# Optimization experiments

Hardware: AMD Instinct MI355X
Metric: run time of the kernel (lower is better)

The kernel has to match this reference:

```python
import jax, jax.numpy as jnp
import numpy as np

N_SEQ, N_RES, C_M = 512, 256, 256
C_OUTER, C_Z = 32, 128
LN_EPS = 1e-5
NORM_EPS = 1e-3


def setup_inputs() -> dict:
    key = jax.random.key(0)
    ks = jax.random.split(key, 6)
    f32 = jnp.float32
    return {
        "act": jax.random.normal(ks[0], (N_SEQ, N_RES, C_M), f32),
        "mask": jnp.ones((N_SEQ, N_RES), f32),
        # LayerNorm params (create_scale=True, create_offset=True)
        "ln_scale": jnp.ones((C_M,), f32),
        "ln_offset": jnp.zeros((C_M,), f32),
        # left/right projections, 'linear' (VarianceScaling fan_in scale=1)
        "left_w": (jax.random.normal(ks[1], (C_M, C_OUTER), f32) / np.float32(np.sqrt(C_M))),
        "left_b": jnp.zeros((C_OUTER,), f32),
        "right_w": (jax.random.normal(ks[2], (C_M, C_OUTER), f32) / np.float32(np.sqrt(C_M))),
        "right_b": jnp.zeros((C_OUTER,), f32),
        # output_w: VarianceScaling(scale=2.0, fan_in) over (c_outer, c_outer) input dims
        "output_w": (jax.random.normal(ks[3], (C_OUTER, C_OUTER, C_Z), f32)
                     * np.float32(np.sqrt(2.0 / (C_OUTER * C_OUTER)))),
        "output_b": jnp.zeros((C_Z,), f32),
    }


def reference(act, mask, ln_scale, ln_offset, left_w, left_b, right_w, right_b,
              output_w, output_b):
    # LayerNorm over last axis
    mu = jnp.mean(act, axis=-1, keepdims=True)
    var = jnp.var(act, axis=-1, keepdims=True)
    x = (act - mu) * jax.lax.rsqrt(var + LN_EPS) * ln_scale + ln_offset

    m = mask[..., None]  # [N_seq, N_res, 1]
    left = m * (jnp.einsum('abm,mc->abc', x, left_w) + left_b)    # [A,B,Co]
    right = m * (jnp.einsum('abm,me->abe', x, right_w) + right_b)  # [A,D,Co]

    # mean outer product: sum over MSA depth a -> [B, D, Co, Co]
    op = jnp.einsum('abc,ade->bdce', left, right)
    out = jnp.einsum('bdce,cef->bdf', op, output_w) + output_b  # [B, D, Cz]

    # normalization by pairwise mask counts
    norm = jnp.einsum('ab,ad->bd', mask, mask)[..., None]  # [B, D, 1]
    return out / (NORM_EPS + norm)
```

## Files before the change

### kernel.cpp

```cpp
#include <hip/hip_runtime.h>
#include <hip/hip_bf16.h>
#include <stdint.h>

typedef short bf16x8 __attribute__((ext_vector_type(8)));
typedef float f32x4 __attribute__((ext_vector_type(4)));
typedef unsigned short u16x4 __attribute__((ext_vector_type(4)));
typedef unsigned short u16x8 __attribute__((ext_vector_type(8)));

#define GLOAD16(g, l) __builtin_amdgcn_global_load_lds( \
    (const __attribute__((address_space(1))) void*)(g), \
    (__attribute__((address_space(3))) void*)(l), 16, 0, 0)

__device__ __forceinline__ unsigned short f2bf(float f) {
  unsigned u = __float_as_uint(f);
  unsigned r = (u + 0x7fffu + ((u >> 16) & 1u)) >> 16;
  return (unsigned short)r;
}

__global__ __launch_bounds__(256) void prep_norm_k(
    const float* __restrict__ lw, const float* __restrict__ rw,
    const float* __restrict__ ow, const float* __restrict__ mask,
    unsigned short* __restrict__ Wt, unsigned short* __restrict__ wfragG,
    float* __restrict__ nrm) {
  const int bid = blockIdx.x;
  if (bid < 512) {
    int idx = bid * 256 + threadIdx.x;
    if (idx < 131072) {
      int f = idx >> 10, k2 = idx & 1023;
      int e = k2 >> 5, c = k2 & 31;
      Wt[idx] = f2bf(ow[(size_t)((c << 5) + e) * 128 + f]);
    }
    if (idx < 16384) {
      int frag = idx >> 9, lane = (idx >> 3) & 63, j = idx & 7;
      int wc = frag >> 4, ni = (frag >> 3) & 1, kk = frag & 7;
      int mrow = lane & 15, g = lane >> 4;
      int c = wc * 32 + ni * 16 + mrow;
      int k = kk * 32 + g * 8 + j;
      wfragG[idx] = f2bf(c < 32 ? lw[k * 32 + c] : rw[k * 32 + (c - 32)]);
    }
  } else {
    const int b = bid - 512, d = threadIdx.x;
    float s = 0.f;
    #pragma unroll 8
    for (int a = 0; a < 512; ++a)
      s += mask[a * 256 + b] * mask[a * 256 + d];
    nrm[(b << 8) + d] = s;
  }
}

__global__ __launch_bounds__(256, 4) void ln_proj(
    const float* __restrict__ act, const float* __restrict__ mask,
    const float* __restrict__ lns, const float* __restrict__ lno,
    const float* __restrict__ lb, const float* __restrict__ rb,
    const unsigned short* __restrict__ wfragG,
    unsigned short* __restrict__ Lt, unsigned short* __restrict__ Rt) {
  __shared__ char smem[32768];
  const int tid = threadIdx.x;
  const int lane = tid & 63;
  const int w = tid >> 6;
  const int b = blockIdx.y;
  const int a0 = blockIdx.x << 6;
  const int l = tid & 15;
  const int rg = tid >> 4;

  f32x4 sc[4], of[4];
  #pragma unroll
  for (int j = 0; j < 4; ++j) {
    sc[j] = *(const f32x4*)(lns + (l << 4) + (j << 2));
    of[j] = *(const f32x4*)(lno + (l << 4) + (j << 2));
  }

  #pragma unroll
  for (int i = 0; i < 4; ++i) {
    const int r = rg + (i << 4);
    const float* src = act + ((size_t)(a0 + r) * 256 + b) * 256 + (l << 4);
    f32x4 xv[4];
    #pragma unroll
    for (int j = 0; j < 4; ++j) xv[j] = *(const f32x4*)(src + (j << 2));
    float s = 0.f, sq = 0.f;
    #pragma unroll
    for (int j = 0; j < 4; ++j) {
      f32x4 v = xv[j];
      s += v[0] + v[1] + v[2] + v[3];
      sq += v[0] * v[0] + v[1] * v[1] + v[2] * v[2] + v[3] * v[3];
    }
    s += __shfl_xor(s, 1); sq += __shfl_xor(sq, 1);
    s += __shfl_xor(s, 2); sq += __shfl_xor(sq, 2);
    s += __shfl_xor(s, 4); sq += __shfl_xor(sq, 4);
    s += __shfl_xor(s, 8); sq += __shfl_xor(sq, 8);
    const float mu = s * (1.f / 256.f);
    const float rs = rsqrtf(sq * (1.f / 256.f) - mu * mu + 1e-5f);
    #pragma unroll
    for (int hh = 0; hh < 2; ++hh) {
      u16x8 pk;
      #pragma unroll
      for (int j2 = 0; j2 < 2; ++j2) {
        const int j = (hh << 1) + j2;
        #pragma unroll
        for (int e = 0; e < 4; ++e)
          pk[(j2 << 2) + e] = f2bf((xv[j][e] - mu) * rs * sc[j][e] + of[j][e]);
      }
      const int c = (l << 1) + hh;
      *(u16x8*)(smem + (r << 9) + ((c ^ (r & 7)) << 4)) = pk;
    }
  }
  __syncthreads();

  const int wr = w >> 1, wc = w & 1;
  const int mrow = lane & 15, g = lane >> 4;
  f32x4 acc[2][2];
  #pragma unroll
  for (int i = 0; i < 2; ++i)
    #pragma unroll
    for (int jj = 0; jj < 2; ++jj) acc[i][jj] = (f32x4){0.f, 0.f, 0.f, 0.f};
  #pragma unroll
  for (int kk = 0; kk < 8; ++kk) {
    bf16x8 af[2], bfr[2];
    #pragma unroll
    for (int mi = 0; mi < 2; ++mi) {
      const int row = (wr << 5) + (mi << 4) + mrow;
      af[mi] = *(const bf16x8*)(smem + (row << 9) + ((((kk << 2) + g) ^ (row & 7)) << 4));
    }
    #pragma unroll
    for (int ni = 0; ni < 2; ++ni)
      bfr[ni] = *(const bf16x8*)(wfragG + (size_t)((((wc << 1) + ni) << 3) + kk) * 512 + (lane << 3));
    #pragma unroll
    for (int mi = 0; mi < 2; ++mi)
      #pragma unroll
      for (int ni = 0; ni < 2; ++ni)
        acc[mi][ni] = __builtin_amdgcn_mfma_f32_16x16x32_bf16(af[mi], bfr[ni], acc[mi][ni], 0, 0, 0);
  }
  __syncthreads();

  #pragma unroll
  for (int ni = 0; ni < 2; ++ni) {
    const int c = (wc << 5) + (ni << 4) + mrow;
    const float bias = (wc == 0) ? lb[(ni << 4) + mrow] : rb[(ni << 4) + mrow];
    #pragma unroll
    for (int mi = 0; mi < 2; ++mi) {
      const int aB = (wr << 5) + (mi << 4) + (g << 2);
      u16x4 pk;
      #pragma unroll
      for (int qq = 0; qq < 4; ++qq) {
        const float mk = mask[(size_t)(a0 + aB + qq) * 256 + b];
        pk[qq] = f2bf((acc[mi][ni][qq] + bias) * mk);
      }
      *(u16x4*)(smem + (c << 7) + ((((aB >> 3) & 7) ^ (c & 7)) << 4) + ((aB & 7) << 1)) = pk;
    }
  }
  __syncthreads();

  #pragma unroll
  for (int s = 0; s < 2; ++s) {
    const int c = (w << 4) + (s << 3) + (lane >> 3);
    const int gr = lane & 7;
    const u16x8 v = *(const u16x8*)(smem + (c << 7) + ((gr ^ (c & 7)) << 4));
    unsigned short* dst = (c < 32) ? Lt : Rt;
    *(u16x8*)(dst + (size_t)(b * 32 + (c & 31)) * 512 + a0 + (gr << 3)) = v;
  }
}

__global__ __launch_bounds__(512, 2) void gemm_fused(
    const unsigned short* __restrict__ Lt, const unsigned short* __restrict__ Rt,
    const unsigned short* __restrict__ Wt, const float* __restrict__ nrm,
    const float* __restrict__ outb, float* __restrict__ out) {
  __shared__ char smem[131072];
  const int tid = threadIdx.x;
  const int lane = tid & 63;
  const int w = tid >> 6;
  const int wr = w >> 2, wc = w & 3;
  const int mrow = lane & 15, g = lane >> 4;

  const int bid = blockIdx.x;
  const int xcd = bid & 7, jj_ = bid >> 3;
  const int mb = ((jj_ >> 5) << 3) | (jj_ & 7);
  const int nb = (xcd << 2) | ((jj_ >> 3) & 3);
  const int m0i = mb << 8, n0i = nb << 8;

  const int scol = (((tid & 7) ^ ((tid >> 3) & 7)) << 3);

  f32x4 acc[8][4];
  #pragma unroll
  for (int i = 0; i < 8; ++i)
    #pragma unroll
    for (int jj = 0; jj < 4; ++jj) acc[i][jj] = (f32x4){0.f, 0.f, 0.f, 0.f};

  auto STG = [&](const unsigned short* gsrc, int baserow, int dstoff, int kt) {
    GLOAD16(gsrc + ((size_t)(baserow + (tid >> 3)) << 9) + (kt << 6) + scol,
            smem + dstoff + (tid << 4));
  };
  auto STGALL = [&](int buf, int kt) {
    STG(Rt, n0i, buf + 32768, kt);        STG(Rt, n0i + 64, buf + 40960, kt);
    STG(Rt, n0i + 128, buf + 49152, kt);  STG(Rt, n0i + 192, buf + 57344, kt);
    STG(Lt, m0i, buf + 0, kt);            STG(Lt, m0i + 64, buf + 8192, kt);
    STG(Lt, m0i + 128, buf + 16384, kt);  STG(Lt, m0i + 192, buf + 24576, kt);
  };

  STGALL(0, 0);
  STGALL(65536, 1);
  asm volatile("s_waitcnt vmcnt(8)" ::: "memory");
  __builtin_amdgcn_s_barrier();

  #pragma unroll 1
  for (int t = 0; t < 8; ++t) {
    const char* bufp = smem + ((t & 1) << 16);
    #pragma unroll
    for (int kk = 0; kk < 2; ++kk) {
      bf16x8 af[8], bfv[4];
      #pragma unroll
      for (int mi = 0; mi < 8; ++mi) {
        const int row = (wr << 7) + (mi << 4) + mrow;
        af[mi] = *(const bf16x8*)(bufp + (row << 7) +
                                  ((((kk << 2) + g) ^ (row & 7)) << 4));
      }
      #pragma unroll
      for (int ni = 0; ni < 4; ++ni) {
        const int row = (wc << 6) + (ni << 4) + mrow;
        bfv[ni] = *(const bf16x8*)(bufp + 32768 + (row << 7) +
                                   ((((kk << 2) + g) ^ (row & 7)) << 4));
      }
      #pragma unroll
      for (int mi = 0; mi < 8; ++mi)
        #pragma unroll
        for (int ni = 0; ni < 4; ++ni)
          acc[mi][ni] = __builtin_amdgcn_mfma_f32_16x16x32_bf16(
              af[mi], bfv[ni], acc[mi][ni], 0, 0, 0);
    }
    if (t < 6) {
      __builtin_amdgcn_s_barrier();
      STGALL((t & 1) << 16, t + 2);
      asm volatile("s_waitcnt vmcnt(8)" ::: "memory");
      __builtin_amdgcn_s_barrier();
    } else if (t == 6) {
      asm volatile("s_waitcnt vmcnt(0)" ::: "memory");
      __builtin_amdgcn_s_barrier();
    }
  }
  __syncthreads();

  #pragma unroll
  for (int mi = 0; mi < 8; ++mi) {
    #pragma unroll
    for (int ni = 0; ni < 4; ++ni) {
      const int p = (((wr << 2) + (mi >> 1)) << 3) | ((wc << 1) + (ni >> 1));
      const int ow_ = ((ni & 1) << 10) + (mrow << 6) + ((mi & 1) << 5) + (g << 3);
      u16x4 pk;
      #pragma unroll
      for (int qq = 0; qq < 4; ++qq) pk[qq] = f2bf(acc[mi][ni][qq]);
      *(u16x4*)(smem + (p << 11) + (ow_ ^ ((p & 7) << 4) ^ (((ow_ >> 7) & 7) << 4))) = pk;
    }
  }
  __syncthreads();

  f32x4 invn[4];
  #pragma unroll
  for (int pg = 0; pg < 4; ++pg) {
    const int bb = (mb << 3) + (pg << 1) + (g >> 1);
    const f32x4 nv = *(const f32x4*)(nrm + (bb << 8) + (nb << 3) + ((g & 1) << 2));
    #pragma unroll
    for (int qq = 0; qq < 4; ++qq) invn[pg][qq] = __builtin_amdgcn_rcpf(1e-3f + nv[qq]);
  }

  const int f0 = w << 4;
  f32x4 acc2[4];
  #pragma unroll
  for (int i = 0; i < 4; ++i) acc2[i] = (f32x4){0.f, 0.f, 0.f, 0.f};
  const unsigned short* wrow = Wt + (size_t)(f0 + mrow) * 1024;
  #pragma unroll 8
  for (int kk2 = 0; kk2 < 32; ++kk2) {
    const bf16x8 b2 = *(const bf16x8*)(wrow + (kk2 << 5) + (g << 3));
    const int orr = (kk2 << 6) + (g << 4);
    #pragma unroll
    for (int pg = 0; pg < 4; ++pg) {
      const int prow = (pg << 4) + mrow;
      const bf16x8 a2 = *(const bf16x8*)(smem + (prow << 11) +
          (orr ^ ((prow & 7) << 4) ^ (((orr >> 7) & 7) << 4)));
      acc2[pg] = __builtin_amdgcn_mfma_f32_16x16x32_bf16(a2, b2, acc2[pg], 0, 0, 0);
    }
  }

  const float ob_ = outb[f0 + mrow];
  #pragma unroll
  for (int pg = 0; pg < 4; ++pg) {
    #pragma unroll
    for (int qq = 0; qq < 4; ++qq) {
      const int p = (pg << 4) + (g << 2) + qq;
      const int bb = (mb << 3) + (p >> 3);
      const int dd = (nb << 3) + (p & 7);
      out[(size_t)((bb << 8) + dd) * 128 + f0 + mrow] = (acc2[pg][qq] + ob_) * invn[pg][qq];
    }
  }
}

extern "C" void kernel_launch(void* const* d_in, const int* in_sizes, int n_in,
                              void* d_out, int out_size, void* d_ws, size_t ws_size,
                              hipStream_t stream) {
  const float* act = (const float*)d_in[0];
  const float* mask = (const float*)d_in[1];
  const float* lns = (const float*)d_in[2];
  const float* lno = (const float*)d_in[3];
  const float* lw = (const float*)d_in[4];
  const float* lb = (const float*)d_in[5];
  const float* rw = (const float*)d_in[6];
  const float* rbv = (const float*)d_in[7];
  const float* ow = (const float*)d_in[8];
  const float* ob = (const float*)d_in[9];
  float* out = (float*)d_out;
  char* ws = (char*)d_ws;

  unsigned short* Lt = (unsigned short*)(ws);
  unsigned short* Rt = (unsigned short*)(ws + 8388608);
  unsigned short* Wt = (unsigned short*)(ws + 16777216);
  unsigned short* wfragG = (unsigned short*)(ws + 17039360);
  float* nrm = (float*)(ws + 17072128);

  hipLaunchKernelGGL(prep_norm_k, dim3(768), dim3(256), 0, stream,
                     lw, rw, ow, mask, Wt, wfragG, nrm);
  hipLaunchKernelGGL(ln_proj, dim3(8, 256), dim3(256), 0, stream,
                     act, mask, lns, lno, lb, rbv, wfragG, Lt, Rt);
  hipLaunchKernelGGL(gemm_fused, dim3(1024), dim3(512), 0, stream,
                     Lt, Rt, Wt, nrm, ob, out);
}
```

Measured before the change: 151.3 us.

## Halve ln_proj tile to 32 rows, remap warps, and prioritize MFMA in GEMM

ln_proj now processes 32 MSA rows per block instead of 64, launches twice as many blocks, and shrinks shared memory so more blocks can be resident. Each thread now normalizes a full row slice with 8 threads per row. Each warp computes one 16-column slice of the projection, and the weight fragment layout is reordered to match. The transpose-out stage uses a small separate LDS buffer. In the main GEMM, B fragments are loaded before A, and s_setprio raises wave priority around the MFMA block. The aim is better occupancy and latency hiding in the memory-bound LN stage, at the cost of reading each wfragG fragment more times overall.

```diff
diff --git a/kernel.cpp b/kernel.cpp
--- a/kernel.cpp
+++ b/kernel.cpp
@@ -32,9 +32,9 @@
     }
     if (idx < 16384) {
       int frag = idx >> 9, lane = (idx >> 3) & 63, j = idx & 7;
-      int wc = frag >> 4, ni = (frag >> 3) & 1, kk = frag & 7;
+      int cw = frag >> 3, kk = frag & 7;
       int mrow = lane & 15, g = lane >> 4;
-      int c = wc * 32 + ni * 16 + mrow;
+      int c = cw * 16 + mrow;
       int k = kk * 32 + g * 8 + j;
       wfragG[idx] = f2bf(c < 32 ? lw[k * 32 + c] : rw[k * 32 + (c - 32)]);
     }
@@ -48,115 +48,98 @@
   }
 }
 
-__global__ __launch_bounds__(256, 4) void ln_proj(
+__global__ __launch_bounds__(256, 6) void ln_proj(
     const float* __restrict__ act, const float* __restrict__ mask,
     const float* __restrict__ lns, const float* __restrict__ lno,
     const float* __restrict__ lb, const float* __restrict__ rb,
     const unsigned short* __restrict__ wfragG,
     unsigned short* __restrict__ Lt, unsigned short* __restrict__ Rt) {
-  __shared__ char smem[32768];
+  __shared__ char smem[16384];
+  __shared__ char tsm[4096];
   const int tid = threadIdx.x;
   const int lane = tid & 63;
   const int w = tid >> 6;
   const int b = blockIdx.y;
-  const int a0 = blockIdx.x << 6;
-  const int l = tid & 15;
-  const int rg = tid >> 4;
-
-  f32x4 sc[4], of[4];
-  #pragma unroll
-  for (int j = 0; j < 4; ++j) {
-    sc[j] = *(const f32x4*)(lns + (l << 4) + (j << 2));
-    of[j] = *(const f32x4*)(lno + (l << 4) + (j << 2));
-  }
-
-  #pragma unroll
-  for (int i = 0; i < 4; ++i) {
-    const int r = rg + (i << 4);
-    const float* src = act + ((size_t)(a0 + r) * 256 + b) * 256 + (l << 4);
-    f32x4 xv[4];
-    #pragma unroll
-    for (int j = 0; j < 4; ++j) xv[j] = *(const f32x4*)(src + (j << 2));
-    float s = 0.f, sq = 0.f;
-    #pragma unroll
-    for (int j = 0; j < 4; ++j) {
-      f32x4 v = xv[j];
-      s += v[0] + v[1] + v[2] + v[3];
-      sq += v[0] * v[0] + v[1] * v[1] + v[2] * v[2] + v[3] * v[3];
-    }
-    s += __shfl_xor(s, 1); sq += __shfl_xor(sq, 1);
-    s += __shfl_xor(s, 2); sq += __shfl_xor(sq, 2);
-    s += __shfl_xor(s, 4); sq += __shfl_xor(sq, 4);
-    s += __shfl_xor(s, 8); sq += __shfl_xor(sq, 8);
-    const float mu = s * (1.f / 256.f);
-    const float rs = rsqrtf(sq * (1.f / 256.f) - mu * mu + 1e-5f);
-    #pragma unroll
-    for (int hh = 0; hh < 2; ++hh) {
-      u16x8 pk;
-      #pragma unroll
-      for (int j2 = 0; j2 < 2; ++j2) {
-        const int j = (hh << 1) + j2;
-        #pragma unroll
-        for (int e = 0; e < 4; ++e)
-          pk[(j2 << 2) + e] = f2bf((xv[j][e] - mu) * rs * sc[j][e] + of[j][e]);
+  const int a0 = blockIdx.x << 5;
+  const int r = tid >> 3;
+  const int q = tid & 7;
+
+  f32x4 xv[8];
+  const float* src = act + ((size_t)(a0 + r) * 256 + b) * 256 + (q << 5);
+  #pragma unroll
+  for (int j = 0; j < 8; ++j) xv[j] = *(const f32x4*)(src + (j << 2));
+  float s = 0.f, sq = 0.f;
+  #pragma unroll
+  for (int j = 0; j < 8; ++j) {
+    f32x4 v = xv[j];
+    s += v[0] + v[1] + v[2] + v[3];
+    sq += v[0] * v[0] + v[1] * v[1] + v[2] * v[2] + v[3] * v[3];
+  }
+  s += __shfl_xor(s, 1); sq += __shfl_xor(sq, 1);
+  s += __shfl_xor(s, 2); sq += __shfl_xor(sq, 2);
+  s += __shfl_xor(s, 4); sq += __shfl_xor(sq, 4);
+  const float mu = s * (1.f / 256.f);
+  const float rs = rsqrtf(sq * (1.f / 256.f) - mu * mu + 1e-5f);
+
+  #pragma unroll
+  for (int cc = 0; cc < 4; ++cc) {
+    u16x8 pk;
+    #pragma unroll
+    for (int h = 0; h < 2; ++h) {
+      const int j = (cc << 1) + h;
+      const f32x4 sc = *(const f32x4*)(lns + (q << 5) + (j << 2));
+      const f32x4 of = *(const f32x4*)(lno + (q << 5) + (j << 2));
+      #pragma unroll
+      for (int e = 0; e < 4; ++e)
+        pk[(h << 2) + e] = f2bf((xv[j][e] - mu) * rs * sc[e] + of[e]);
+    }
+    const int c = (q << 2) + cc;
+    *(u16x8*)(smem + (r << 9) + ((c ^ (r & 7)) << 4)) = pk;
+  }
+  __syncthreads();
+
+  const int mrow = lane & 15, g = lane >> 4;
+  f32x4 acc[2];
+  acc[0] = (f32x4){0.f, 0.f, 0.f, 0.f};
+  acc[1] = (f32x4){0.f, 0.f, 0.f, 0.f};
+  #pragma unroll
+  for (int kk = 0; kk < 8; ++kk) {
+    const bf16x8 bfr = *(const bf16x8*)(wfragG + (size_t)((w << 3) + kk) * 512 + (lane << 3));
+    #pragma unroll
+    for (int mi = 0; mi < 2; ++mi) {
+      const int row = (mi << 4) + mrow;
+      const bf16x8 af = *(const bf16x8*)(smem + (row << 9) + ((((kk << 2) + g) ^ (row & 7)) << 4));
+      acc[mi] = __builtin_amdgcn_mfma_f32_16x16x32_bf16(af, bfr, acc[mi], 0, 0, 0);
+    }
+  }
+
+  {
+    const int c = (w << 4) + mrow;
+    const float bias = (c < 32) ? lb[c] : rb[c - 32];
+    #pragma unroll
+    for (int mi = 0; mi < 2; ++mi) {
+      const int abase = (mi << 4) + (g << 2);
+      u16x4 pk;
+      #pragma unroll
+      for (int qq = 0; qq < 4; ++qq) {
+        const float mk = mask[(size_t)(a0 + abase + qq) * 256 + b];
+        pk[qq] = f2bf((acc[mi][qq] + bias) * mk);
       }
-      const int c = (l << 1) + hh;
-      *(u16x8*)(smem + (r << 9) + ((c ^ (r & 7)) << 4)) = pk;
+      const int sl = abase >> 2;
+      *(u16x4*)(tsm + (c << 6) + ((sl ^ (c & 7)) << 3)) = pk;
     }
   }
   __syncthreads();
 
-  const int wr = w >> 1, wc = w & 1;
-  const int mrow = lane & 15, g = lane >> 4;
-  f32x4 acc[2][2];
-  #pragma unroll
-  for (int i = 0; i < 2; ++i)
-    #pragma unroll
-    for (int jj = 0; jj < 2; ++jj) acc[i][jj] = (f32x4){0.f, 0.f, 0.f, 0.f};
-  #pragma unroll
-  for (int kk = 0; kk < 8; ++kk) {
-    bf16x8 af[2], bfr[2];
-    #pragma unroll
-    for (int mi = 0; mi < 2; ++mi) {
-      const int row = (wr << 5) + (mi << 4) + mrow;
-      af[mi] = *(const bf16x8*)(smem + (row << 9) + ((((kk << 2) + g) ^ (row & 7)) << 4));
-    }
-    #pragma unroll
-    for (int ni = 0; ni < 2; ++ni)
-      bfr[ni] = *(const bf16x8*)(wfragG + (size_t)((((wc << 1) + ni) << 3) + kk) * 512 + (lane << 3));
-    #pragma unroll
-    for (int mi = 0; mi < 2; ++mi)
-      #pragma unroll
-      for (int ni = 0; ni < 2; ++ni)
-        acc[mi][ni] = __builtin_amdgcn_mfma_f32_16x16x32_bf16(af[mi], bfr[ni], acc[mi][ni], 0, 0, 0);
-  }
-  __syncthreads();
-
-  #pragma unroll
-  for (int ni = 0; ni < 2; ++ni) {
-    const int c = (wc << 5) + (ni << 4) + mrow;
-    const float bias = (wc == 0) ? lb[(ni << 4) + mrow] : rb[(ni << 4) + mrow];
-    #pragma unroll
-    for (int mi = 0; mi < 2; ++mi) {
-      const int aB = (wr << 5) + (mi << 4) + (g << 2);
-      u16x4 pk;
-      #pragma unroll
-      for (int qq = 0; qq < 4; ++qq) {
-        const float mk = mask[(size_t)(a0 + aB + qq) * 256 + b];
-        pk[qq] = f2bf((acc[mi][ni][qq] + bias) * mk);
-      }
-      *(u16x4*)(smem + (c << 7) + ((((aB >> 3) & 7) ^ (c & 7)) << 4) + ((aB & 7) << 1)) = pk;
-    }
-  }
-  __syncthreads();
-
-  #pragma unroll
-  for (int s = 0; s < 2; ++s) {
-    const int c = (w << 4) + (s << 3) + (lane >> 3);
-    const int gr = lane & 7;
-    const u16x8 v = *(const u16x8*)(smem + (c << 7) + ((gr ^ (c & 7)) << 4));
+  {
+    const int c = tid >> 2, q2 = tid & 3;
+    const u16x4 lo = *(const u16x4*)(tsm + (c << 6) + ((((q2 << 1) + 0) ^ (c & 7)) << 3));
+    const u16x4 hi = *(const u16x4*)(tsm + (c << 6) + ((((q2 << 1) + 1) ^ (c & 7)) << 3));
+    u16x8 v;
+    #pragma unroll
+    for (int e = 0; e < 4; ++e) { v[e] = lo[e]; v[e + 4] = hi[e]; }
     unsigned short* dst = (c < 32) ? Lt : Rt;
-    *(u16x8*)(dst + (size_t)(b * 32 + (c & 31)) * 512 + a0 + (gr << 3)) = v;
+    *(u16x8*)(dst + (size_t)(b * 32 + (c & 31)) * 512 + a0 + (q2 << 3)) = v;
   }
 }
 
@@ -208,23 +191,25 @@
     for (int kk = 0; kk < 2; ++kk) {
       bf16x8 af[8], bfv[4];
       #pragma unroll
+      for (int ni = 0; ni < 4; ++ni) {
+        const int row = (wc << 6) + (ni << 4) + mrow;
+        bfv[ni] = *(const bf16x8*)(bufp + 32768 + (row << 7) +
+                                   ((((kk << 2) + g) ^ (row & 7)) << 4));
+      }
+      #pragma unroll
       for (int mi = 0; mi < 8; ++mi) {
         const int row = (wr << 7) + (mi << 4) + mrow;
         af[mi] = *(const bf16x8*)(bufp + (row << 7) +
                                   ((((kk << 2) + g) ^ (row & 7)) << 4));
       }
-      #pragma unroll
-      for (int ni = 0; ni < 4; ++ni) {
-        const int row = (wc << 6) + (ni << 4) + mrow;
-        bfv[ni] = *(const bf16x8*)(bufp + 32768 + (row << 7) +
-                                   ((((kk << 2) + g) ^ (row & 7)) << 4));
-      }
+      __builtin_amdgcn_s_setprio(1);
       #pragma unroll
       for (int mi = 0; mi < 8; ++mi)
         #pragma unroll
         for (int ni = 0; ni < 4; ++ni)
           acc[mi][ni] = __builtin_amdgcn_mfma_f32_16x16x32_bf16(
               af[mi], bfv[ni], acc[mi][ni], 0, 0, 0);
+      __builtin_amdgcn_s_setprio(0);
     }
     if (t < 6) {
       __builtin_amdgcn_s_barrier();
@@ -316,7 +301,7 @@
 
   hipLaunchKernelGGL(prep_norm_k, dim3(768), dim3(256), 0, stream,
                      lw, rw, ow, mask, Wt, wfragG, nrm);
-  hipLaunchKernelGGL(ln_proj, dim3(8, 256), dim3(256), 0, stream,
+  hipLaunchKernelGGL(ln_proj, dim3(16, 256), dim3(256), 0, stream,
                      act, mask, lns, lno, lb, rbv, wfragG, Lt, Rt);
   hipLaunchKernelGGL(gemm_fused, dim3(1024), dim3(512), 0, stream,
                      Lt, Rt, Wt, nrm, ob, out);
```

Result: slower. 175.6 us (+16.0%).
